# Kernel tuning notes

Hardware: AMD Instinct MI355X
Metric: run time of the kernel (lower is better)

The kernel has to match this reference:

```python
import jax, jax.numpy as jnp
import numpy as np

B, N, C_IN, FC0, K = 16, 32768, 32, 256, 1024
CHUNK = 64  # chunk over the K=1024 attention channels to bound the [N,CHUNK,C] intermediate
BN_EPS = 1e-5


def _lengths():
    rng = np.random.default_rng(0)
    r = rng.integers(1024, 3072, size=B)
    l = (r * N) // r.sum()
    l[-1] += N - l.sum()
    assert l.min() > 0 and l.sum() == N
    return jnp.asarray(l, dtype=jnp.int32)


def setup_inputs() -> dict:
    key = jax.random.key(0)
    ks = jax.random.split(key, 16)
    f32 = jnp.float32
    x = jax.random.normal(ks[0], (N, C_IN), dtype=f32)
    # conv1d_1 (1x1 conv == per-point linear), BN1
    w1 = jax.random.normal(ks[1], (FC0, C_IN), dtype=f32) * 0.1
    b1 = jax.random.normal(ks[2], (FC0,), dtype=f32) * 0.1
    g1 = 1.0 + 0.1 * jax.random.normal(ks[3], (FC0,), dtype=f32)
    be1 = 0.1 * jax.random.normal(ks[4], (FC0,), dtype=f32)
    m1 = 0.1 * jax.random.normal(ks[5], (FC0,), dtype=f32)
    v1 = 0.5 + jax.random.uniform(ks[6], (FC0,), dtype=f32)
    # conv1d_2, BN2
    w2 = jax.random.normal(ks[7], (K, FC0), dtype=f32) * 0.05
    b2 = jax.random.normal(ks[8], (K,), dtype=f32) * 0.1
    g2 = 1.0 + 0.1 * jax.random.normal(ks[9], (K,), dtype=f32)
    be2 = 0.1 * jax.random.normal(ks[10], (K,), dtype=f32)
    m2 = 0.1 * jax.random.normal(ks[11], (K,), dtype=f32)
    v2 = 0.5 + jax.random.uniform(ks[12], (K,), dtype=f32)
    # fc_1, BN3
    fcw = jax.random.normal(ks[13], (FC0, C_IN * K), dtype=f32) * 0.01
    fcb = jax.random.normal(ks[14], (FC0,), dtype=f32) * 0.1
    kb = jax.random.split(ks[15], 4)
    g3 = 1.0 + 0.1 * jax.random.normal(kb[0], (FC0,), dtype=f32)
    be3 = 0.1 * jax.random.normal(kb[1], (FC0,), dtype=f32)
    m3 = 0.1 * jax.random.normal(kb[2], (FC0,), dtype=f32)
    v3 = 0.5 + jax.random.uniform(kb[3], (FC0,), dtype=f32)
    return dict(x=x, length=_lengths(), w1=w1, b1=b1, g1=g1, be1=be1, m1=m1, v1=v1,
                w2=w2, b2=b2, g2=g2, be2=be2, m2=m2, v2=v2,
                fcw=fcw, fcb=fcb, g3=g3, be3=be3, m3=m3, v3=v3)


def _bn(x, g, b, m, v):
    # eval-mode BatchNorm (running stats)
    return (x - m) * (g * jax.lax.rsqrt(v + BN_EPS)) + b


def _forward(x, length, w1, b1, g1, be1, m1, v1, w2, b2, g2, be2, m2, v2,
             fcw, fcb, g3, be3, m3, v3):
    # attention features: conv1x1 -> BN -> ReLU, twice  -> [N, K]
    att = jax.nn.relu(_bn(x @ w1.T + b1, g1, be1, m1, v1))
    att = jax.nn.relu(_bn(att @ w2.T + b2, g2, be2, m2, v2))

    seg = jnp.repeat(jnp.arange(B, dtype=jnp.int32), length, total_repeat_length=N)  # [N]

    # per-segment softmax over the point axis (torch F.softmax(..., dim=0))
    mx = jax.ops.segment_max(att, seg, num_segments=B)              # [B, K]
    e = jnp.exp(att - mx[seg])
    w = e / jax.ops.segment_sum(e, seg, num_segments=B)[seg]        # [N, K]

    # per-segment weighted pooling: out[b] = att_b.T @ x_b, chunked over K
    chunks = []
    for s in range(0, K, CHUNK):
        contrib = w[:, s:s + CHUNK, None] * x[:, None, :]           # [N, CHUNK, C]
        chunks.append(jax.ops.segment_sum(contrib, seg, num_segments=B))
    pooled = jnp.concatenate(chunks, axis=1)                        # [B, K, C]
    pooled = pooled / length[:, None, None].astype(x.dtype)
    out2 = pooled.reshape(B, K * C_IN)                              # row-major flatten of [K, C]

    r = _bn(out2 @ fcw.T + fcb, g3, be3, m3, v3)                    # [B, 256]
    # F.normalize(p=2, dim=1, eps=1e-12)
    return r / jnp.maximum(jnp.linalg.norm(r, axis=1, keepdims=True), 1e-12)


def reference(x, length, w1, b1, g1, be1, m1, v1, w2, b2, g2, be2, m2, v2,
              fcw, fcb, g3, be3, m3, v3):
    return _forward(x, length, w1, b1, g1, be1, m1, v1, w2, b2, g2, be2, m2, v2,
                    fcw, fcb, g3, be3, m3, v3)
```

## Files before the change

### kernel.cpp

```cpp
#include <hip/hip_runtime.h>
#include <hip/hip_bf16.h>

typedef __bf16 bf16x8 __attribute__((ext_vector_type(8)));
typedef float f32x4 __attribute__((ext_vector_type(4)));
typedef unsigned long long ull;

__device__ inline unsigned short f2bf(float f) {
    unsigned u = __builtin_bit_cast(unsigned, f);
    unsigned r = (u + 0x7fffu + ((u >> 16) & 1u)) >> 16;
    return (unsigned short)r;
}
__device__ inline float bf2f(unsigned short h) {
    unsigned u = ((unsigned)h) << 16;
    return __builtin_bit_cast(float, u);
}

__device__ inline void gload_lds16(const void* g, void* l) {
    __builtin_amdgcn_global_load_lds((const __attribute__((address_space(1))) void*)g,
                                     (__attribute__((address_space(3))) void*)l, 16, 0, 0);
}

#define MAXCH 272

__global__ __launch_bounds__(256) void k01_prep_gemm1(const float* __restrict__ x,
                                                      const float* __restrict__ w1,
                                                      const float* __restrict__ b1,
                                                      const float* __restrict__ g1,
                                                      const float* __restrict__ be1,
                                                      const float* __restrict__ m1,
                                                      const float* __restrict__ v1,
                                                      const float* __restrict__ w2,
                                                      const int* __restrict__ length,
                                                      unsigned short* __restrict__ w2p,
                                                      int* __restrict__ meta,
                                                      unsigned short* __restrict__ att1) {
    int tid = threadIdx.x;
    int i = blockIdx.x * 256 + tid;
    if (i < 32768) {
        int kb = i >> 9, kk = (i >> 6) & 7, l = i & 63;
        int col = kb * 16 + (l & 15);
        int kin = kk * 32 + (l >> 4) * 8;
        unsigned short v[8];
#pragma unroll
        for (int j = 0; j < 8; j++) v[j] = f2bf(w2[(size_t)col * 256 + kin + j]);
        *(ull*)(w2p + (size_t)i * 8)     = *(ull*)&v[0];
        *(ull*)(w2p + (size_t)i * 8 + 4) = *(ull*)&v[4];
    }
    if (blockIdx.x == 0 && tid < 64) {
        int lane = tid;
        int b = lane & 15;
        int len = length[b];
        int off = 0, chbase = 0, nch = 0;
        int nchb = (len + 127) >> 7;
#pragma unroll
        for (int j = 0; j < 16; j++) {
            int lj = __shfl(len, j, 64);
            int nj = __shfl(nchb, j, 64);
            if (j < b) { off += lj; chbase += nj; }
            nch += nj;
        }
        int total = __shfl(off + len, 15, 64);
        if (lane < 16) {
            meta[b] = off;
            meta[848 + b] = chbase;
            meta[864 + b] = chbase + nchb;
            if (b == 0) { meta[16] = total; meta[17] = nch; }
            for (int t = 0; t < nchb; t++) {
                int s = off + t * 128;
                int en = off + len < s + 128 ? off + len : s + 128;
                meta[304 + chbase + t] = s;
                meta[576 + chbase + t] = en;
            }
        }
    }
    __shared__ float xs[64][33];
    int row0 = blockIdx.x * 64;
    for (int ii = tid; ii < 64 * 32; ii += 256) {
        int rr = ii >> 5, c = ii & 31;
        xs[rr][c] = x[(row0 + rr) * 32 + c];
    }
    __syncthreads();
    int j = tid;
    float w[32];
#pragma unroll
    for (int c = 0; c < 32; c++) w[c] = w1[j * 32 + c];
    float s = g1[j] * rsqrtf(v1[j] + 1e-5f);
    float bias = (b1[j] - m1[j]) * s + be1[j];
    for (int rr = 0; rr < 64; rr++) {
        float acc = 0.f;
#pragma unroll
        for (int c = 0; c < 32; c++) acc = fmaf(xs[rr][c], w[c], acc);
        float t = fmaf(acc, s, bias);
        att1[(row0 + rr) * 256 + j] = f2bf(fmaxf(t, 0.f));
    }
}

__global__ __launch_bounds__(256, 2) void k23_fused(const unsigned short* __restrict__ att1,
                                                    const unsigned short* __restrict__ w2p,
                                                    const float* __restrict__ x,
                                                    const int* __restrict__ meta,
                                                    const float* __restrict__ b2,
                                                    const float* __restrict__ g2,
                                                    const float* __restrict__ be2,
                                                    const float* __restrict__ m2,
                                                    const float* __restrict__ v2,
                                                    float* __restrict__ pP,
                                                    float* __restrict__ pS) {
    __shared__ __align__(16) unsigned short As[2][128 * 64];
    __shared__ __align__(16) unsigned short xT[48 * 128];
    int flat = blockIdx.x;
    int xcd = flat & 7, q = flat >> 3;
    int ch = (q >> 3) * 8 + xcd;
    int kt = q & 7;
    if (ch >= meta[17]) return;
    int n0 = meta[304 + ch];
    int rows = meta[576 + ch] - n0;
    int col0 = kt * 128;
    int tid = threadIdx.x, lane = tid & 63, wave = tid >> 6;
    int lr = lane & 15, s16 = lane >> 4;
    int wr = wave >> 1, wc = wave & 1;

    auto stage = [&](int t, int buf) {
#pragma unroll
        for (int it = 0; it < 4; it++) {
            int idx = it * 256 + tid;
            int row = idx >> 3, slot = idx & 7;
            int srow = row < rows ? row : rows - 1;
            int g = slot ^ (row & 7);
            gload_lds16(att1 + (size_t)(n0 + srow) * 256 + t * 64 + g * 8,
                        (char*)As + buf * 16384 + it * 4096 + wave * 1024);
        }
    };

    int kb0 = kt * 8 + wc * 4;
    auto loadB = [&](int t, bf16x8 (&bb)[2][4]) {
#pragma unroll
        for (int kk = 0; kk < 2; kk++)
#pragma unroll
            for (int n = 0; n < 4; n++)
                bb[kk][n] = *(const bf16x8*)(const void*)(
                    w2p + (size_t)(((kb0 + n) * 8 + t * 2 + kk) * 64 + lane) * 8);
    };

    bf16x8 b0[2][4], b1[2][4];
    stage(0, 0);
    loadB(0, b0);

#pragma unroll
    for (int p = 0; p < 8; p++) {
        int nb = p * 16 + (tid >> 5) * 2;
        int c = tid & 31;
        float v0 = (nb < rows) ? x[(size_t)(n0 + nb) * 32 + c] : 0.f;
        float v1 = (nb + 1 < rows) ? x[(size_t)(n0 + nb + 1) * 32 + c] : 0.f;
        unsigned pk = ((unsigned)f2bf(v1) << 16) | f2bf(v0);
        int byte = c * 256 + ((nb * 2) ^ ((c & 15) << 4));
        *(unsigned*)((char*)xT + byte) = pk;
    }
    if (tid < 128) {
        int byte = 32 * 256 + tid * 2;
        *(unsigned short*)((char*)xT + byte) = (tid < rows) ? f2bf(1.f) : (unsigned short)0;
    }
    __syncthreads();

    f32x4 acc[4][4] = {};
#pragma unroll
    for (int t = 0; t < 4; t++) {
        if (t < 3) stage(t + 1, (t & 1) ^ 1);
        if (t == 0) loadB(1, b1);
        else if (t == 1) loadB(2, b0);
        else if (t == 2) loadB(3, b1);
        const char* Ab = (const char*)As + (t & 1) * 16384;
#pragma unroll
        for (int kk = 0; kk < 2; kk++) {
            bf16x8 a[4];
#pragma unroll
            for (int m = 0; m < 4; m++) {
                int row = wr * 64 + m * 16 + lr;
                int slot = (kk * 4 + s16) ^ (row & 7);
                a[m] = *(const bf16x8*)(const void*)(Ab + row * 128 + slot * 16);
            }
#pragma unroll
            for (int m = 0; m < 4; m++)
#pragma unroll
                for (int n = 0; n < 4; n++)
                    acc[m][n] = __builtin_amdgcn_mfma_f32_16x16x32_bf16(
                        a[m], (t & 1) ? b1[kk][n] : b0[kk][n], acc[m][n], 0, 0, 0);
        }
        __syncthreads();
    }

    char* eT = (char*)As;
#pragma unroll
    for (int nf = 0; nf < 4; nf++) {
        int k = wc * 64 + nf * 16 + lr;
        int kg = col0 + k;
        float sc = g2[kg] * rsqrtf(v2[kg] + 1e-5f);
        float bias = (b2[kg] - m2[kg]) * sc + be2[kg];
#pragma unroll
        for (int m = 0; m < 4; m++) {
            int nbase = wr * 64 + m * 16 + s16 * 4;
            ull pk = 0;
#pragma unroll
            for (int rg = 0; rg < 4; rg++) {
                float tt = fmaf(acc[m][nf][rg], sc, bias);
                float ev = __expf(fmaxf(tt, 0.f));
                unsigned short h = (nbase + rg < rows) ? f2bf(ev) : (unsigned short)0;
                pk |= ((ull)h) << (16 * rg);
            }
            int byte = k * 256 + ((nbase * 2) ^ ((k & 15) << 4));
            *(ull*)(eT + byte) = pk;
        }
    }
    __syncthreads();

    f32x4 pacc[2][3] = {};
#pragma unroll
    for (int nc = 0; nc < 128; nc += 32) {
        bf16x8 ea[2], xb[3];
#pragma unroll
        for (int i = 0; i < 2; i++) {
            int k = (wave * 2 + i) * 16 + lr;
            int byte = k * 256 + (((nc + s16 * 8) * 2) ^ ((k & 15) << 4));
            ea[i] = *(const bf16x8*)(const void*)(eT + byte);
        }
#pragma unroll
        for (int j = 0; j < 3; j++) {
            int c = j * 16 + lr;
            int byte = c * 256 + (((nc + s16 * 8) * 2) ^ ((c & 15) << 4));
            xb[j] = *(const bf16x8*)(const void*)((const char*)xT + byte);
        }
#pragma unroll
        for (int i = 0; i < 2; i++)
#pragma unroll
            for (int j = 0; j < 3; j++)
                pacc[i][j] = __builtin_amdgcn_mfma_f32_16x16x32_bf16(ea[i], xb[j], pacc[i][j], 0, 0, 0);
    }

    float* pPc = pP + (size_t)ch * 32768;
#pragma unroll
    for (int i = 0; i < 2; i++) {
#pragma unroll
        for (int j = 0; j < 3; j++) {
            int c = j * 16 + lr;
#pragma unroll
            for (int rg = 0; rg < 4; rg++) {
                int k = (wave * 2 + i) * 16 + s16 * 4 + rg;
                float v = pacc[i][j][rg];
                if (c < 32) pPc[(col0 + k) * 32 + c] = v;
                else if (c == 32) pS[ch * 1024 + col0 + k] = v;
            }
        }
    }
}

__global__ __launch_bounds__(256) void k3b_reduce(const float* __restrict__ pP,
                                                  const float* __restrict__ pS,
                                                  const int* __restrict__ meta,
                                                  float* __restrict__ out2) {
    int id = blockIdx.x * 256 + threadIdx.x;
    int base = id * 4;
    int b = base >> 15, rem = base & 32767, k = rem >> 5;
    f32x4 P = {0.f, 0.f, 0.f, 0.f};
    float S = 0.f;
    int c0 = meta[848 + b], c1 = meta[864 + b];
    for (int ch = c0; ch < c1; ch++) {
        P += *(const f32x4*)(const void*)(pP + (size_t)ch * 32768 + rem);
        S += pS[ch * 1024 + k];
    }
    float inv = 1.f / (S * (float)(meta[b + 1] - meta[b]));
    *(f32x4*)(void*)(out2 + base) = P * inv;
}

__global__ __launch_bounds__(256) void k4_fc(const float* __restrict__ out2,
                                             const float* __restrict__ fcw,
                                             float* __restrict__ pFC) {
    int jt = blockIdx.x, dc = blockIdx.y;
    int tid = threadIdx.x;
    float acc[16][8] = {};
#pragma unroll
    for (int i = 0; i < 16; i++) {
        int d = dc * 4096 + i * 256 + tid;
        float wv[8];
#pragma unroll
        for (int jj = 0; jj < 8; jj++) wv[jj] = fcw[(size_t)(jt * 8 + jj) * 32768 + d];
#pragma unroll
        for (int bb = 0; bb < 16; bb++) {
            float ov = out2[bb * 32768 + d];
#pragma unroll
            for (int jj = 0; jj < 8; jj++) acc[bb][jj] = fmaf(ov, wv[jj], acc[bb][jj]);
        }
    }
    __shared__ float red[32][257];
#pragma unroll
    for (int p = 0; p < 4; p++) {
#pragma unroll
        for (int q = 0; q < 4; q++)
#pragma unroll
            for (int jj = 0; jj < 8; jj++)
                red[q * 8 + jj][tid] = acc[p * 4 + q][jj];
        __syncthreads();
        int row = tid >> 3, sg = tid & 7;
        float s = 0.f;
        for (int u = sg; u < 256; u += 8) s += red[row][u];
        s += __shfl_down(s, 4, 8);
        s += __shfl_down(s, 2, 8);
        s += __shfl_down(s, 1, 8);
        if (sg == 0) {
            int bb = p * 4 + (row >> 3), jj = row & 7;
            pFC[(dc * 16 + bb) * 256 + jt * 8 + jj] = s;
        }
        __syncthreads();
    }
}

__global__ __launch_bounds__(256) void k45_fc2(const float* __restrict__ pFC,
                                               const float* __restrict__ fcb,
                                               const float* __restrict__ g3,
                                               const float* __restrict__ be3,
                                               const float* __restrict__ m3,
                                               const float* __restrict__ v3,
                                               float* __restrict__ out) {
    int b = blockIdx.x, j = threadIdx.x;
    float sum = 0.f;
#pragma unroll
    for (int dc = 0; dc < 8; dc++) sum += pFC[(dc * 16 + b) * 256 + j];
    float sc = g3[j] * rsqrtf(v3[j] + 1e-5f);
    float rv = (sum + fcb[j] - m3[j]) * sc + be3[j];
    float sq = rv * rv;
#pragma unroll
    for (int o = 32; o > 0; o >>= 1) sq += __shfl_down(sq, o, 64);
    __shared__ float wsum[4];
    if ((j & 63) == 0) wsum[j >> 6] = sq;
    __syncthreads();
    float tot = wsum[0] + wsum[1] + wsum[2] + wsum[3];
    out[b * 256 + j] = rv / fmaxf(sqrtf(tot), 1e-12f);
}

extern "C" void kernel_launch(void* const* d_in, const int* in_sizes, int n_in,
                              void* d_out, int out_size, void* d_ws, size_t ws_size,
                              hipStream_t stream) {
    const float* x    = (const float*)d_in[0];
    const int*   len  = (const int*)d_in[1];
    const float* w1   = (const float*)d_in[2];
    const float* b1   = (const float*)d_in[3];
    const float* g1   = (const float*)d_in[4];
    const float* be1  = (const float*)d_in[5];
    const float* m1   = (const float*)d_in[6];
    const float* v1   = (const float*)d_in[7];
    const float* w2   = (const float*)d_in[8];
    const float* b2   = (const float*)d_in[9];
    const float* g2   = (const float*)d_in[10];
    const float* be2  = (const float*)d_in[11];
    const float* m2   = (const float*)d_in[12];
    const float* v2   = (const float*)d_in[13];
    const float* fcw  = (const float*)d_in[14];
    const float* fcb  = (const float*)d_in[15];
    const float* g3   = (const float*)d_in[16];
    const float* be3  = (const float*)d_in[17];
    const float* m3   = (const float*)d_in[18];
    const float* v3   = (const float*)d_in[19];

    char* ws = (char*)d_ws;
    int* meta            = (int*)ws;
    unsigned short* w2p  = (unsigned short*)(ws + 4096);
    unsigned short* att1 = (unsigned short*)(ws + 528384);
    float* pP            = (float*)(ws + 17305600);
    float* pS            = (float*)(ws + 52957184);
    float* out2          = (float*)(ws + 54071296);
    float* pFC           = (float*)(ws + 56168448);
    float* out           = (float*)d_out;

    hipLaunchKernelGGL(k01_prep_gemm1, dim3(512),       dim3(256), 0, stream,
                       x, w1, b1, g1, be1, m1, v1, w2, len, w2p, meta, att1);
    hipLaunchKernelGGL(k23_fused,  dim3(MAXCH * 8), dim3(256), 0, stream, att1, w2p, x, meta, b2, g2, be2, m2, v2, pP, pS);
    hipLaunchKernelGGL(k3b_reduce, dim3(512),       dim3(256), 0, stream, pP, pS, meta, out2);
    hipLaunchKernelGGL(k4_fc,      dim3(32, 8),     dim3(256), 0, stream, out2, fcw, pFC);
    hipLaunchKernelGGL(k45_fc2,    dim3(16),        dim3(256), 0, stream, pFC, fcb, g3, be3, m3, v3, out);
}
```

Measured before the change: 94.08 us.

## Store pooled partials as bf16 and compute softmax denominators from epilogue row sums

Per-chunk pooled partials are now written to global memory as bf16 instead of fp32. This halves the partial buffer that the reduce kernel must read back. The softmax denominator no longer comes from an extra ones-column MFMA tile. Each wave instead sums its exp values with shuffles and writes two partial sums per chunk, which drops a third of the pooling MFMAs and LDS reads. The reduce kernel now loads eight bf16 values per thread and runs with half the blocks; the cost is extra rounding error in the partials.

```diff
diff --git a/kernel.cpp b/kernel.cpp
--- a/kernel.cpp
+++ b/kernel.cpp
@@ -2,6 +2,7 @@
 #include <hip/hip_bf16.h>
 
 typedef __bf16 bf16x8 __attribute__((ext_vector_type(8)));
+typedef unsigned short u16x8 __attribute__((ext_vector_type(8)));
 typedef float f32x4 __attribute__((ext_vector_type(4)));
 typedef unsigned long long ull;
 
@@ -104,10 +105,10 @@
                                                     const float* __restrict__ be2,
                                                     const float* __restrict__ m2,
                                                     const float* __restrict__ v2,
-                                                    float* __restrict__ pP,
-                                                    float* __restrict__ pS) {
+                                                    unsigned short* __restrict__ pP,
+                                                    float* __restrict__ pS2) {
     __shared__ __align__(16) unsigned short As[2][128 * 64];
-    __shared__ __align__(16) unsigned short xT[48 * 128];
+    __shared__ __align__(16) unsigned short xT[32 * 128];
     int flat = blockIdx.x;
     int xcd = flat & 7, q = flat >> 3;
     int ch = (q >> 3) * 8 + xcd;
@@ -156,10 +157,6 @@
         int byte = c * 256 + ((nb * 2) ^ ((c & 15) << 4));
         *(unsigned*)((char*)xT + byte) = pk;
     }
-    if (tid < 128) {
-        int byte = 32 * 256 + tid * 2;
-        *(unsigned short*)((char*)xT + byte) = (tid < rows) ? f2bf(1.f) : (unsigned short)0;
-    }
     __syncthreads();
 
     f32x4 acc[4][4] = {};
@@ -190,6 +187,7 @@
     }
 
     char* eT = (char*)As;
+    float ssum[4] = {0.f, 0.f, 0.f, 0.f};
 #pragma unroll
     for (int nf = 0; nf < 4; nf++) {
         int k = wc * 64 + nf * 16 + lr;
@@ -205,18 +203,29 @@
                 float tt = fmaf(acc[m][nf][rg], sc, bias);
                 float ev = __expf(fmaxf(tt, 0.f));
                 unsigned short h = (nbase + rg < rows) ? f2bf(ev) : (unsigned short)0;
+                ssum[nf] += bf2f(h);
                 pk |= ((ull)h) << (16 * rg);
             }
             int byte = k * 256 + ((nbase * 2) ^ ((k & 15) << 4));
             *(ull*)(eT + byte) = pk;
         }
     }
+#pragma unroll
+    for (int nf = 0; nf < 4; nf++) {
+        ssum[nf] += __shfl_xor(ssum[nf], 16, 64);
+        ssum[nf] += __shfl_xor(ssum[nf], 32, 64);
+    }
+    if (s16 == 0) {
+#pragma unroll
+        for (int nf = 0; nf < 4; nf++)
+            pS2[ch * 2048 + wr * 1024 + col0 + wc * 64 + nf * 16 + lr] = ssum[nf];
+    }
     __syncthreads();
 
-    f32x4 pacc[2][3] = {};
+    f32x4 pacc[2][2] = {};
 #pragma unroll
     for (int nc = 0; nc < 128; nc += 32) {
-        bf16x8 ea[2], xb[3];
+        bf16x8 ea[2], xb[2];
 #pragma unroll
         for (int i = 0; i < 2; i++) {
             int k = (wave * 2 + i) * 16 + lr;
@@ -224,7 +233,7 @@
             ea[i] = *(const bf16x8*)(const void*)(eT + byte);
         }
 #pragma unroll
-        for (int j = 0; j < 3; j++) {
+        for (int j = 0; j < 2; j++) {
             int c = j * 16 + lr;
             int byte = c * 256 + (((nc + s16 * 8) * 2) ^ ((c & 15) << 4));
             xb[j] = *(const bf16x8*)(const void*)((const char*)xT + byte);
@@ -232,43 +241,46 @@
 #pragma unroll
         for (int i = 0; i < 2; i++)
 #pragma unroll
-            for (int j = 0; j < 3; j++)
+            for (int j = 0; j < 2; j++)
                 pacc[i][j] = __builtin_amdgcn_mfma_f32_16x16x32_bf16(ea[i], xb[j], pacc[i][j], 0, 0, 0);
     }
 
-    float* pPc = pP + (size_t)ch * 32768;
+    unsigned short* pPc = pP + (size_t)ch * 32768;
 #pragma unroll
     for (int i = 0; i < 2; i++) {
 #pragma unroll
-        for (int j = 0; j < 3; j++) {
+        for (int j = 0; j < 2; j++) {
             int c = j * 16 + lr;
 #pragma unroll
             for (int rg = 0; rg < 4; rg++) {
                 int k = (wave * 2 + i) * 16 + s16 * 4 + rg;
-                float v = pacc[i][j][rg];
-                if (c < 32) pPc[(col0 + k) * 32 + c] = v;
-                else if (c == 32) pS[ch * 1024 + col0 + k] = v;
+                pPc[(col0 + k) * 32 + c] = f2bf(pacc[i][j][rg]);
             }
         }
     }
 }
 
-__global__ __launch_bounds__(256) void k3b_reduce(const float* __restrict__ pP,
-                                                  const float* __restrict__ pS,
+__global__ __launch_bounds__(256) void k3b_reduce(const unsigned short* __restrict__ pP,
+                                                  const float* __restrict__ pS2,
                                                   const int* __restrict__ meta,
                                                   float* __restrict__ out2) {
     int id = blockIdx.x * 256 + threadIdx.x;
-    int base = id * 4;
+    int base = id * 8;
     int b = base >> 15, rem = base & 32767, k = rem >> 5;
-    f32x4 P = {0.f, 0.f, 0.f, 0.f};
+    float P[8] = {};
     float S = 0.f;
     int c0 = meta[848 + b], c1 = meta[864 + b];
     for (int ch = c0; ch < c1; ch++) {
-        P += *(const f32x4*)(const void*)(pP + (size_t)ch * 32768 + rem);
-        S += pS[ch * 1024 + k];
+        u16x8 v = *(const u16x8*)(const void*)(pP + (size_t)ch * 32768 + rem);
+#pragma unroll
+        for (int j = 0; j < 8; j++) P[j] += bf2f(v[j]);
+        S += pS2[ch * 2048 + k] + pS2[ch * 2048 + 1024 + k];
     }
     float inv = 1.f / (S * (float)(meta[b + 1] - meta[b]));
-    *(f32x4*)(void*)(out2 + base) = P * inv;
+    f32x4 o0 = {P[0] * inv, P[1] * inv, P[2] * inv, P[3] * inv};
+    f32x4 o1 = {P[4] * inv, P[5] * inv, P[6] * inv, P[7] * inv};
+    *(f32x4*)(void*)(out2 + base) = o0;
+    *(f32x4*)(void*)(out2 + base + 4) = o1;
 }
 
 __global__ __launch_bounds__(256) void k4_fc(const float* __restrict__ out2,
@@ -364,16 +376,16 @@
     int* meta            = (int*)ws;
     unsigned short* w2p  = (unsigned short*)(ws + 4096);
     unsigned short* att1 = (unsigned short*)(ws + 528384);
-    float* pP            = (float*)(ws + 17305600);
-    float* pS            = (float*)(ws + 52957184);
-    float* out2          = (float*)(ws + 54071296);
-    float* pFC           = (float*)(ws + 56168448);
+    unsigned short* pP   = (unsigned short*)(ws + 17305600);
+    float* pS2           = (float*)(ws + 35131392);
+    float* out2          = (float*)(ws + 37359616);
+    float* pFC           = (float*)(ws + 39456768);
     float* out           = (float*)d_out;
 
-    hipLaunchKernelGGL(k01_prep_gemm1, dim3(512),       dim3(256), 0, stream,
+    hipLaunchKernelGGL(k01_prep_gemm1, dim3(512),   dim3(256), 0, stream,
                        x, w1, b1, g1, be1, m1, v1, w2, len, w2p, meta, att1);
-    hipLaunchKernelGGL(k23_fused,  dim3(MAXCH * 8), dim3(256), 0, stream, att1, w2p, x, meta, b2, g2, be2, m2, v2, pP, pS);
-    hipLaunchKernelGGL(k3b_reduce, dim3(512),       dim3(256), 0, stream, pP, pS, meta, out2);
+    hipLaunchKernelGGL(k23_fused,  dim3(MAXCH * 8), dim3(256), 0, stream, att1, w2p, x, meta, b2, g2, be2, m2, v2, pP, pS2);
+    hipLaunchKernelGGL(k3b_reduce, dim3(256),       dim3(256), 0, stream, pP, pS2, meta, out2);
     hipLaunchKernelGGL(k4_fc,      dim3(32, 8),     dim3(256), 0, stream, out2, fcw, pFC);
     hipLaunchKernelGGL(k45_fc2,    dim3(16),        dim3(256), 0, stream, pFC, fcb, g3, be3, m3, v3, out);
 }
```

Result: slower. 97.00 us (+3.1%).
